# Performance work log

Measured on AMD Instinct MI355X. Metric: run time of the kernel, lower is better.

Reference implementation:

```python
import jax, jax.numpy as jnp
import numpy as np

H = 96  # hidden_dim


def _rbf(dist):
    # GaussianSmearing(start=0, stop=10, num_gaussians=16)
    offset = jnp.linspace(0.0, 10.0, 16, dtype=dist.dtype)
    coeff = -0.5 / (10.0 / 15.0) ** 2
    d = dist[:, None] - offset[None, :]
    return jnp.exp(coeff * d * d)


def _gatv2(s, edge, edge_attr, Wl, bl, Wr, br, We, att, bias):
    # PyG GATv2Conv, heads=1: e = leaky_relu(lin_l(x_src)+lin_r(x_tgt)+lin_edge(ea));
    # alpha = segment_softmax(e @ att, tgt); out = scatter_sum(alpha * lin_l(x_src)) + bias
    N = s.shape[0]
    src, tgt = edge[0], edge[1]
    xl = s @ Wl + bl
    xr = s @ Wr + br
    e = jax.nn.leaky_relu(xl[src] + xr[tgt] + edge_attr @ We, 0.2)  # [E,H]
    logits = e @ att  # [E]
    m = jax.ops.segment_max(logits, tgt, num_segments=N)
    a = jnp.exp(logits - m[tgt])
    denom = jax.ops.segment_sum(a, tgt, num_segments=N)
    alpha = a / denom[tgt]
    out = jax.ops.segment_sum(alpha[:, None] * xl[src], tgt, num_segments=N)
    return out + bias


def _encoder(x, edge, pos, Wemb, bemb, gp):
    s0 = x @ Wemb + bemb                      # [N,H]
    s = jax.nn.silu(s0)
    row, col = edge[0], edge[1]
    dist = jnp.linalg.norm(pos[row] - pos[col], axis=-1)
    ea = _rbf(dist)                           # [E,16]
    s = s + jax.nn.silu(_gatv2(s, edge, ea, *gp))
    v = s0.reshape(x.shape[0], -1, 3)[:, :16, :]  # [N,16,3]
    return s, v


def _forward(x_L, pos_L, x_P, pos_P, edge_L, edge_P, cross_src, cross_tgt,
             Wemb_L, bemb_L, Wl_L, bl_L, Wr_L, br_L, We_L, att_L, bias_L,
             Wemb_P, bemb_P, Wl_P, bl_P, Wr_P, br_P, We_P, att_P, bias_P,
             Win, b_in, Wout, bout, Wq, bq, Wk, bk, Wv, bv, W1, b1, W2, b2):
    s_L, v_L = _encoder(x_L, edge_L, pos_L, Wemb_L, bemb_L,
                        (Wl_L, bl_L, Wr_L, br_L, We_L, att_L, bias_L))
    s_P, v_P = _encoder(x_P, edge_P, pos_P, Wemb_P, bemb_P,
                        (Wl_P, bl_P, Wr_P, br_P, We_P, att_P, bias_P))
    # CausalMolSSM: x + out_proj(silu(in_proj(x)).chunk(2)[0])
    h = jax.nn.silu(s_L @ Win + b_in)[:, : 2 * H]
    s_L = s_L + h @ Wout + bout
    # GVPCrossAttention: per-edge gather, global softmax (dim=0 in source), scatter-add
    q = (s_L @ Wq + bq)[cross_tgt]
    k = (s_P @ Wk + bk)[cross_src]
    logits = jnp.sum(q * k, axis=-1) / 8.0     # [E_X]
    attn = jax.nn.softmax(logits, axis=0)      # global softmax over all edges (as in source)
    vmsg = (s_P @ Wv + bv)[cross_src]
    s_L = s_L.at[cross_tgt].add(attn[:, None] * vmsg)
    # head
    return jax.nn.silu(s_L @ W1 + b1) @ W2 + b2  # v_pred [N_L,3]


def setup_inputs() -> dict:
    N_L, N_P = 8192, 32768
    E_L, E_P, E_X = 262144, 524288, 262144
    D_L, D_P = 167, 21
    ks = iter(jax.random.split(jax.random.key(0), 64))

    def w(shape, fan):
        return (jax.random.normal(next(ks), shape, dtype=jnp.float32) / np.sqrt(fan)).astype(jnp.float32)

    inp = {}
    inp['x_L'] = jax.random.normal(next(ks), (N_L, D_L), dtype=jnp.float32)
    inp['pos_L'] = jax.random.normal(next(ks), (N_L, 3), dtype=jnp.float32)
    inp['x_P'] = jax.random.normal(next(ks), (N_P, D_P), dtype=jnp.float32)
    inp['pos_P'] = jax.random.normal(next(ks), (N_P, 3), dtype=jnp.float32)
    inp['edge_L'] = jax.random.randint(next(ks), (2, E_L), 0, N_L)
    inp['edge_P'] = jax.random.randint(next(ks), (2, E_P), 0, N_P)
    inp['cross_src'] = jax.random.randint(next(ks), (E_X,), 0, N_P)
    inp['cross_tgt'] = jax.random.randint(next(ks), (E_X,), 0, N_L)
    for pre, din in (('L', D_L), ('P', D_P)):
        inp[f'Wemb_{pre}'] = w((din, H), din); inp[f'bemb_{pre}'] = w((H,), din)
        inp[f'Wl_{pre}'] = w((H, H), H); inp[f'bl_{pre}'] = w((H,), H)
        inp[f'Wr_{pre}'] = w((H, H), H); inp[f'br_{pre}'] = w((H,), H)
        inp[f'We_{pre}'] = w((16, H), 16)
        inp[f'att_{pre}'] = w((H,), H)
        inp[f'bias_{pre}'] = w((H,), H)
    inp['Win'] = w((H, 4 * H), H); inp['b_in'] = w((4 * H,), H)
    inp['Wout'] = w((2 * H, H), 2 * H); inp['bout'] = w((H,), 2 * H)
    for n in ('q', 'k', 'v'):
        inp[f'W{n}'] = w((H, H), H); inp[f'b{n}'] = w((H,), H)
    inp['W1'] = w((H, H), H); inp['b1'] = w((H,), H)
    inp['W2'] = w((H, 3), H); inp['b2'] = w((3,), H)
    return inp


def reference(x_L, pos_L, x_P, pos_P, edge_L, edge_P, cross_src, cross_tgt,
              Wemb_L, bemb_L, Wl_L, bl_L, Wr_L, br_L, We_L, att_L, bias_L,
              Wemb_P, bemb_P, Wl_P, bl_P, Wr_P, br_P, We_P, att_P, bias_P,
              Win, b_in, Wout, bout, Wq, bq, Wk, bk, Wv, bv, W1, b1, W2, b2):
    return _forward(x_L, pos_L, x_P, pos_P, edge_L, edge_P, cross_src, cross_tgt,
                    Wemb_L, bemb_L, Wl_L, bl_L, Wr_L, br_L, We_L, att_L, bias_L,
                    Wemb_P, bemb_P, Wl_P, bl_P, Wr_P, br_P, We_P, att_P, bias_P,
                    Win, b_in, Wout, bout, Wq, bq, Wk, bk, Wv, bv, W1, b1, W2, b2)
```

## Files before the change

kernel.cpp:

```cpp
#include <hip/hip_runtime.h>

__device__ __forceinline__ float silu_f(float x) { return x / (1.f + __expf(-x)); }

__device__ __forceinline__ void atomicMaxF(float* addr, float val) {
    if (val >= 0.f) atomicMax((int*)addr, __float_as_int(val));
    else            atomicMin((unsigned int*)addr, __float_as_uint(val));
}

__device__ __forceinline__ unsigned short f2bf(float x) {
    unsigned int u = __float_as_uint(x);
    return (unsigned short)((u + 0x7fffu + ((u >> 16) & 1u)) >> 16);
}
__device__ __forceinline__ float bf2f(unsigned short h) {
    return __uint_as_float(((unsigned int)h) << 16);
}
__device__ __forceinline__ float bf_lo(unsigned int u) { return __uint_as_float(u << 16); }
__device__ __forceinline__ float bf_hi(unsigned int u) { return __uint_as_float(u & 0xffff0000u); }
__device__ __forceinline__ float bfdot(unsigned int a, unsigned int b) {
    return bf_lo(a) * bf_lo(b) + bf_hi(a) * bf_hi(b);
}

__global__ void fill_i(int* __restrict__ p, int v, int n) {
    int i = blockIdx.x * blockDim.x + threadIdx.x;
    if (i < n) p[i] = v;
}

__global__ __launch_bounds__(256) void hist_all_kernel(const int* __restrict__ tgtL,
        const int* __restrict__ tgtP, const int* __restrict__ ctgt, int* __restrict__ count,
        int E_L, int E_P, int E_X, int N_L, int N_P) {
    int e = blockIdx.x * blockDim.x + threadIdx.x;
    if (e < E_L) atomicAdd(&count[tgtL[e]], 1);
    else if (e < E_L + E_P) atomicAdd(&count[N_L + tgtP[e - E_L]], 1);
    else if (e < E_L + E_P + E_X) atomicAdd(&count[N_L + N_P + ctgt[e - E_L - E_P]], 1);
}

__global__ __launch_bounds__(256) void scan_blocksum_kernel(const int* __restrict__ count,
                                                            int* __restrict__ bsum, int n) {
    int b = blockIdx.x, t = threadIdx.x;
    int base = b * 4096 + t * 16;
    int s = 0;
#pragma unroll
    for (int k = 0; k < 16; ++k) {
        int idx = base + k;
        s += (idx < n) ? count[idx] : 0;
    }
#pragma unroll
    for (int off = 1; off < 64; off <<= 1) s += __shfl_xor(s, off, 64);
    __shared__ int ws[4];
    int lane = t & 63, wid = t >> 6;
    if (lane == 0) ws[wid] = s;
    __syncthreads();
    if (t == 0) bsum[b] = ws[0] + ws[1] + ws[2] + ws[3];
}

__global__ void scan_top_kernel(int* __restrict__ bsum, int nb, float* __restrict__ csc) {
    if (threadIdx.x == 0) {
        int run = 0;
        for (int i = 0; i < nb; ++i) { int c = bsum[i]; bsum[i] = run; run += c; }
        csc[0] = -3.4e38f; csc[1] = 0.f;
    }
}

__global__ __launch_bounds__(256) void scan_apply_kernel(const int* __restrict__ count,
        const int* __restrict__ bsum, int* __restrict__ rowptr, int* __restrict__ cursor,
        int n, int E) {
    int b = blockIdx.x, t = threadIdx.x;
    int base = b * 4096 + t * 16;
    int v[16];
    int s = 0;
#pragma unroll
    for (int k = 0; k < 16; ++k) {
        int idx = base + k;
        v[k] = (idx < n) ? count[idx] : 0;
        s += v[k];
    }
    int lane = t & 63, wid = t >> 6;
    int inc = s;
#pragma unroll
    for (int off = 1; off < 64; off <<= 1) {
        int o = __shfl_up(inc, off, 64);
        if (lane >= off) inc += o;
    }
    __shared__ int ws[4];
    if (lane == 63) ws[wid] = inc;
    __syncthreads();
    int woff = 0;
    for (int w = 0; w < wid; ++w) woff += ws[w];
    int prefix = bsum[b] + woff + (inc - s);
#pragma unroll
    for (int k = 0; k < 16; ++k) {
        int idx = base + k;
        if (idx < n) { rowptr[idx] = prefix; cursor[idx] = prefix; prefix += v[k]; }
    }
    if (b == 0 && t == 0) rowptr[n] = E;
}

__global__ __launch_bounds__(256) void pre_all_kernel(const int* __restrict__ eL,
        const int* __restrict__ eP, const int* __restrict__ csrc, const int* __restrict__ ctgt,
        const float* __restrict__ posL, const float* __restrict__ posP,
        int* __restrict__ cursor, unsigned int* __restrict__ sdp,
        int E_L, int E_P, int E_X, int N_L, int N_P) {
    int e = blockIdx.x * blockDim.x + threadIdx.x;
    if (e >= E_L + E_P + E_X) return;
    unsigned int pack;
    int node;
    if (e < E_L + E_P) {
        const int* ed; const float* pos; int idx, E, nbase;
        if (e < E_L) { ed = eL; pos = posL; idx = e; E = E_L; nbase = 0; }
        else         { ed = eP; pos = posP; idx = e - E_L; E = E_P; nbase = N_L; }
        int si = ed[idx], ti = ed[E + idx];
        node = nbase + ti;
        float dx = pos[si * 3 + 0] - pos[ti * 3 + 0];
        float dy = pos[si * 3 + 1] - pos[ti * 3 + 1];
        float dz = pos[si * 3 + 2] - pos[ti * 3 + 2];
        float dist = sqrtf(dx * dx + dy * dy + dz * dz);
        int dq = min((int)(dist * 4096.f), 65535);
        pack = (unsigned int)(si + nbase) | ((unsigned int)dq << 16);
    } else {
        int idx = e - E_L - E_P;
        int ti = ctgt[idx];
        pack = (unsigned int)csrc[idx] | ((unsigned int)ti << 16);
        node = N_L + N_P + ti;
    }
    int p = atomicAdd(&cursor[node], 1);
    sdp[p] = pack;
}

__global__ __launch_bounds__(96) void rbf_table_pack_kernel(const float* __restrict__ We_L,
        const float* __restrict__ We_P, unsigned int* __restrict__ T2_L,
        unsigned int* __restrict__ T2_P) {
    int b = blockIdx.x;
    const float* We = (b < 1024) ? We_L : We_P;
    unsigned int* T2 = (b < 1024) ? T2_L : T2_P;
    int i = (b < 1024) ? b : b - 1024;
    int h = threadIdx.x;
    float d0 = (float)i * 0.015625f, d1 = (float)(i + 1) * 0.015625f;
    float a0 = 0.f, a1 = 0.f;
#pragma unroll
    for (int g = 0; g < 16; ++g) {
        float w = We[g * 96 + h];
        float t0 = d0 - 0.66666667f * (float)g;
        float t1 = d1 - 0.66666667f * (float)g;
        a0 += __expf(-1.125f * t0 * t0) * w;
        a1 += __expf(-1.125f * t1 * t1) * w;
    }
    T2[i * 96 + h] = (unsigned int)f2bf(a0) | ((unsigned int)f2bf(a1 - a0) << 16);
}

__global__ __launch_bounds__(256) void gat_all_kernel(const int* __restrict__ rowptr,
        const unsigned int* __restrict__ sdp, const unsigned short* __restrict__ xlb,
        const unsigned short* __restrict__ xrb,
        const unsigned int* __restrict__ T2_L, const unsigned int* __restrict__ T2_P,
        const float* __restrict__ att_L, const float* __restrict__ att_P,
        const float* __restrict__ bias_L, const float* __restrict__ bias_P,
        float* __restrict__ s_L, float* __restrict__ s_P, int N_L, int Ncomb) {
    int tid = threadIdx.x;
    int l = tid & 31;
    int n = blockIdx.x * 8 + (tid >> 5);
    if (n >= Ncomb) return;
    bool isL = n < N_L;
    const unsigned int* T2 = isL ? T2_L : T2_P;
    const float* att = isL ? att_L : att_P;
    const float* bias = isL ? bias_L : bias_P;
    float* srow = isL ? (s_L + (size_t)n * 96) : (s_P + (size_t)(n - N_L) * 96);
    float att0 = att[l], att1 = att[32 + l], att2 = att[64 + l];
    size_t nb = (size_t)n * 96;
    float xr0 = bf2f(xrb[nb + l]), xr1 = bf2f(xrb[nb + 32 + l]), xr2 = bf2f(xrb[nb + 64 + l]);
    int beg = rowptr[n], end = rowptr[n + 1];
    float m = -3.4e38f, d = 0.f, a0 = 0.f, a1 = 0.f, a2 = 0.f;
    for (int j = beg; j < end; j += 4) {
        unsigned int tp0[4], tp1[4], tp2[4];
        unsigned short xs0[4], xs1[4], xs2[4];
        float ff[4];
#pragma unroll
        for (int k = 0; k < 4; ++k) {
            int jj = min(j + k, end - 1);
            unsigned int u = sdp[jj];
            int src = (int)(u & 0xffffu);
            int dq = (int)(u >> 16);
            int i = dq >> 6;
            ff[k] = (float)(dq & 63) * 0.015625f;
            const unsigned int* tr = T2 + (size_t)i * 96;
            tp0[k] = tr[l]; tp1[k] = tr[32 + l]; tp2[k] = tr[64 + l];
            const unsigned short* xp = xlb + (size_t)src * 96;
            xs0[k] = xp[l]; xs1[k] = xp[32 + l]; xs2[k] = xp[64 + l];
        }
        float y0[4], y1[4], y2[4], lt[4];
#pragma unroll
        for (int k = 0; k < 4; ++k) {
            y0[k] = bf2f(xs0[k]); y1[k] = bf2f(xs1[k]); y2[k] = bf2f(xs2[k]);
            float v0 = y0[k] + xr0 + bf_lo(tp0[k]) + ff[k] * bf_hi(tp0[k]);
            float v1 = y1[k] + xr1 + bf_lo(tp1[k]) + ff[k] * bf_hi(tp1[k]);
            float v2 = y2[k] + xr2 + bf_lo(tp2[k]) + ff[k] * bf_hi(tp2[k]);
            v0 = fmaxf(v0, 0.f) + 0.2f * fminf(v0, 0.f);
            v1 = fmaxf(v1, 0.f) + 0.2f * fminf(v1, 0.f);
            v2 = fmaxf(v2, 0.f) + 0.2f * fminf(v2, 0.f);
            float t = v0 * att0 + v1 * att1 + v2 * att2;
#pragma unroll
            for (int off = 1; off < 32; off <<= 1) t += __shfl_xor(t, off, 64);
            lt[k] = (j + k < end) ? t : -3.4e38f;
        }
        float bm = fmaxf(fmaxf(lt[0], lt[1]), fmaxf(lt[2], lt[3]));
        float nm = fmaxf(m, bm);
        float sc = __expf(m - nm);
        d *= sc; a0 *= sc; a1 *= sc; a2 *= sc;
#pragma unroll
        for (int k = 0; k < 4; ++k) {
            float w = __expf(lt[k] - nm);
            d += w;
            a0 += w * y0[k]; a1 += w * y1[k]; a2 += w * y2[k];
        }
        m = nm;
    }
    float agg0 = (d > 0.f) ? a0 / d : 0.f;
    float agg1 = (d > 0.f) ? a1 / d : 0.f;
    float agg2 = (d > 0.f) ? a2 / d : 0.f;
    srow[l]      += silu_f(agg0 + bias[l]);
    srow[32 + l] += silu_f(agg1 + bias[32 + l]);
    srow[64 + l] += silu_f(agg2 + bias[64 + l]);
}

__global__ __launch_bounds__(256) void cross_logit_e_kernel(const unsigned int* __restrict__ sdX,
        const unsigned short* __restrict__ qnb, const unsigned short* __restrict__ knb,
        float* __restrict__ clog_s, float* __restrict__ csc, int E) {
    int e = blockIdx.x * blockDim.x + threadIdx.x;
    float logit = -3.4e38f;
    if (e < E) {
        unsigned int u = sdX[e];
        int src = (int)(u & 0xffffu);
        int tgt = (int)(u >> 16);
        const uint4* q4 = (const uint4*)(qnb + (size_t)tgt * 96);
        const uint4* k4 = (const uint4*)(knb + (size_t)src * 96);
        float acc = 0.f;
#pragma unroll
        for (int i = 0; i < 12; ++i) {
            uint4 qa = q4[i], ka = k4[i];
            acc += bfdot(qa.x, ka.x) + bfdot(qa.y, ka.y) + bfdot(qa.z, ka.z) + bfdot(qa.w, ka.w);
        }
        logit = acc * 0.125f;
        clog_s[e] = logit;
    }
    __shared__ float red[256];
    red[threadIdx.x] = logit; __syncthreads();
    for (int s = 128; s > 0; s >>= 1) {
        if (threadIdx.x < s) red[threadIdx.x] = fmaxf(red[threadIdx.x], red[threadIdx.x + s]);
        __syncthreads();
    }
    if (threadIdx.x == 0) atomicMaxF(&csc[0], red[0]);
}

__global__ __launch_bounds__(256) void cross_denom_kernel(const float* __restrict__ clog_s,
                                                          float* __restrict__ csc, int E) {
    int e = blockIdx.x * blockDim.x + threadIdx.x;
    float a = 0.f;
    float mg = csc[0];
    if (e < E) a = __expf(clog_s[e] - mg);
    __shared__ float red[256];
    red[threadIdx.x] = a; __syncthreads();
    for (int s = 128; s > 0; s >>= 1) {
        if (threadIdx.x < s) red[threadIdx.x] += red[threadIdx.x + s];
        __syncthreads();
    }
    if (threadIdx.x == 0) atomicAdd(&csc[1], red[0]);
}

__global__ __launch_bounds__(256) void cross_apply_v4_kernel(const int* __restrict__ rowptr,
        const unsigned int* __restrict__ sdp, const float* __restrict__ clog_s,
        const unsigned short* __restrict__ vnb, const float* __restrict__ csc,
        float* __restrict__ sL, int N, int baseX) {
    int tid = threadIdx.x;
    int l = tid & 31;
    int n = blockIdx.x * 8 + (tid >> 5);
    if (n >= N) return;
    int beg = rowptr[n], end = rowptr[n + 1];
    if (beg == end) return;
    float M = csc[0], invD = 1.f / csc[1];
    float a0 = 0.f, a1 = 0.f, a2 = 0.f;
    for (int j = beg; j < end; j += 4) {
        unsigned short v0[4], v1[4], v2[4]; float w[4];
#pragma unroll
        for (int k = 0; k < 4; ++k) {
            int jj = min(j + k, end - 1);
            int src = (int)(sdp[jj] & 0xffffu);
            const unsigned short* vp = vnb + (size_t)src * 96;
            v0[k] = vp[l]; v1[k] = vp[32 + l]; v2[k] = vp[64 + l];
            w[k] = (j + k < end) ? __expf(clog_s[jj - baseX] - M) : 0.f;
        }
#pragma unroll
        for (int k = 0; k < 4; ++k) {
            a0 += w[k] * bf2f(v0[k]); a1 += w[k] * bf2f(v1[k]); a2 += w[k] * bf2f(v2[k]);
        }
    }
    size_t nb = (size_t)n * 96;
    sL[nb + l]      += a0 * invD;
    sL[nb + 32 + l] += a1 * invD;
    sL[nb + 64 + l] += a2 * invD;
}


__global__ __launch_bounds__(192) void enc_all_kernel(
        const float* __restrict__ x_L, const float* __restrict__ x_P,
        const float* __restrict__ WembL, const float* __restrict__ bembL,
        const float* __restrict__ WembP, const float* __restrict__ bembP,
        const float* __restrict__ WlL, const float* __restrict__ blL,
        const float* __restrict__ WrL, const float* __restrict__ brL,
        const float* __restrict__ WlP, const float* __restrict__ blP,
        const float* __restrict__ WrP, const float* __restrict__ brP,
        float* __restrict__ s_L, float* __restrict__ s_P,
        unsigned short* __restrict__ xlb, unsigned short* __restrict__ xrb,
        int N_L, int N_P, int D_L, int D_P, int BL) {
    __shared__ float xs[32 * 167];
    __shared__ float ss[32 * 96];
    int b = blockIdx.x;
    bool isL = b < BL;
    const float* x    = isL ? x_L : x_P;
    const float* Wemb = isL ? WembL : WembP;
    const float* bemb = isL ? bembL : bembP;
    const float* Wl   = isL ? WlL : WlP;
    const float* bl   = isL ? blL : blP;
    const float* Wr   = isL ? WrL : WrP;
    const float* br   = isL ? brL : brP;
    float* sOut = isL ? s_L : s_P;
    int N = isL ? N_L : N_P;
    int D = isL ? D_L : D_P;
    int n0 = (isL ? b : b - BL) * 32;
    int cbase = isL ? 0 : N_L;
    int t = threadIdx.x;
    int hg = t % 24, h4 = hg * 4;
    int rg = t / 24;
    for (int i = t; i < 32 * D; i += 192) {
        int r = i / D, dd = i - r * D, nn = n0 + r;
        xs[i] = (nn < N) ? x[(size_t)nn * D + dd] : 0.f;
    }
    __syncthreads();
    float4 be = *(const float4*)&bemb[h4];
    float acc[4][4];
#pragma unroll
    for (int r = 0; r < 4; ++r) { acc[r][0] = be.x; acc[r][1] = be.y; acc[r][2] = be.z; acc[r][3] = be.w; }
    const float* xrow = &xs[rg * 4 * D];
    for (int dd = 0; dd < D; ++dd) {
        float4 w = *(const float4*)&Wemb[dd * 96 + h4];
#pragma unroll
        for (int r = 0; r < 4; ++r) {
            float xv = xrow[r * D + dd];
            acc[r][0] += xv * w.x; acc[r][1] += xv * w.y;
            acc[r][2] += xv * w.z; acc[r][3] += xv * w.w;
        }
    }
#pragma unroll
    for (int r = 0; r < 4; ++r) {
        int row = rg * 4 + r, nn = n0 + row;
        float4 v = make_float4(silu_f(acc[r][0]), silu_f(acc[r][1]),
                               silu_f(acc[r][2]), silu_f(acc[r][3]));
        *(float4*)&ss[row * 96 + h4] = v;
        if (nn < N) *(float4*)&sOut[(size_t)nn * 96 + h4] = v;
    }
    __syncthreads();
    float4 b1v = *(const float4*)&bl[h4];
    float4 b2v = *(const float4*)&br[h4];
    float a1[4][4], a2[4][4];
#pragma unroll
    for (int r = 0; r < 4; ++r) {
        a1[r][0] = b1v.x; a1[r][1] = b1v.y; a1[r][2] = b1v.z; a1[r][3] = b1v.w;
        a2[r][0] = b2v.x; a2[r][1] = b2v.y; a2[r][2] = b2v.z; a2[r][3] = b2v.w;
    }
    const float* srow = &ss[rg * 4 * 96];
    for (int k = 0; k < 96; ++k) {
        float4 w1 = *(const float4*)&Wl[k * 96 + h4];
        float4 w2 = *(const float4*)&Wr[k * 96 + h4];
#pragma unroll
        for (int r = 0; r < 4; ++r) {
            float xv = srow[r * 96 + k];
            a1[r][0] += xv * w1.x; a1[r][1] += xv * w1.y; a1[r][2] += xv * w1.z; a1[r][3] += xv * w1.w;
            a2[r][0] += xv * w2.x; a2[r][1] += xv * w2.y; a2[r][2] += xv * w2.z; a2[r][3] += xv * w2.w;
        }
    }
#pragma unroll
    for (int r = 0; r < 4; ++r) {
        int nn = n0 + rg * 4 + r;
        if (nn < N) {
            size_t o = (size_t)(cbase + nn) * 96 + h4;
            *(ushort4*)&xlb[o] = make_ushort4(f2bf(a1[r][0]), f2bf(a1[r][1]), f2bf(a1[r][2]), f2bf(a1[r][3]));
            *(ushort4*)&xrb[o] = make_ushort4(f2bf(a2[r][0]), f2bf(a2[r][1]), f2bf(a2[r][2]), f2bf(a2[r][3]));
        }
    }
}

__global__ __launch_bounds__(192) void qkv_all_kernel(
        const float* __restrict__ s_L, const float* __restrict__ s_P,
        const float* __restrict__ Wq, const float* __restrict__ bq,
        const float* __restrict__ Wk, const float* __restrict__ bk,
        const float* __restrict__ Wv, const float* __restrict__ bv,
        unsigned short* __restrict__ qnb, unsigned short* __restrict__ knb,
        unsigned short* __restrict__ vnb, int N_L, int N_P, int BL) {
    __shared__ float xs[32 * 96];
    int b = blockIdx.x;
    bool isL = b < BL;
    const float* s = isL ? s_L : s_P;
    int N = isL ? N_L : N_P;
    int n0 = (isL ? b : b - BL) * 32;
    int t = threadIdx.x;
    int hg = t % 24, h4 = hg * 4;
    int rg = t / 24;
    for (int i = t; i < 32 * 96; i += 192) {
        int r = i / 96, c = i - r * 96, nn = n0 + r;
        xs[i] = (nn < N) ? s[(size_t)nn * 96 + c] : 0.f;
    }
    __syncthreads();
    const float* srow = &xs[rg * 4 * 96];
    if (isL) {
        float4 bb = *(const float4*)&bq[h4];
        float a1[4][4];
#pragma unroll
        for (int r = 0; r < 4; ++r) { a1[r][0] = bb.x; a1[r][1] = bb.y; a1[r][2] = bb.z; a1[r][3] = bb.w; }
        for (int k = 0; k < 96; ++k) {
            float4 w = *(const float4*)&Wq[k * 96 + h4];
#pragma unroll
            for (int r = 0; r < 4; ++r) {
                float xv = srow[r * 96 + k];
                a1[r][0] += xv * w.x; a1[r][1] += xv * w.y; a1[r][2] += xv * w.z; a1[r][3] += xv * w.w;
            }
        }
#pragma unroll
        for (int r = 0; r < 4; ++r) {
            int nn = n0 + rg * 4 + r;
            if (nn < N)
                *(ushort4*)&qnb[(size_t)nn * 96 + h4] =
                    make_ushort4(f2bf(a1[r][0]), f2bf(a1[r][1]), f2bf(a1[r][2]), f2bf(a1[r][3]));
        }
    } else {
        float4 bb1 = *(const float4*)&bk[h4];
        float4 bb2 = *(const float4*)&bv[h4];
        float a1[4][4], a2[4][4];
#pragma unroll
        for (int r = 0; r < 4; ++r) {
            a1[r][0] = bb1.x; a1[r][1] = bb1.y; a1[r][2] = bb1.z; a1[r][3] = bb1.w;
            a2[r][0] = bb2.x; a2[r][1] = bb2.y; a2[r][2] = bb2.z; a2[r][3] = bb2.w;
        }
        for (int k = 0; k < 96; ++k) {
            float4 w1 = *(const float4*)&Wk[k * 96 + h4];
            float4 w2 = *(const float4*)&Wv[k * 96 + h4];
#pragma unroll
            for (int r = 0; r < 4; ++r) {
                float xv = srow[r * 96 + k];
                a1[r][0] += xv * w1.x; a1[r][1] += xv * w1.y; a1[r][2] += xv * w1.z; a1[r][3] += xv * w1.w;
                a2[r][0] += xv * w2.x; a2[r][1] += xv * w2.y; a2[r][2] += xv * w2.z; a2[r][3] += xv * w2.w;
            }
        }
#pragma unroll
        for (int r = 0; r < 4; ++r) {
            int nn = n0 + rg * 4 + r;
            if (nn < N) {
                *(ushort4*)&knb[(size_t)nn * 96 + h4] =
                    make_ushort4(f2bf(a1[r][0]), f2bf(a1[r][1]), f2bf(a1[r][2]), f2bf(a1[r][3]));
                *(ushort4*)&vnb[(size_t)nn * 96 + h4] =
                    make_ushort4(f2bf(a2[r][0]), f2bf(a2[r][1]), f2bf(a2[r][2]), f2bf(a2[r][3]));
            }
        }
    }
}

__global__ __launch_bounds__(192) void ssm3_kernel(float* __restrict__ sL,
        const float* __restrict__ Win, const float* __restrict__ b_in,
        const float* __restrict__ Wout, const float* __restrict__ bout, int N) {
    __shared__ float row[8 * 96];
    __shared__ float u[8 * 192];
    int t = threadIdx.x;
    int n0 = blockIdx.x * 8;
    for (int i = t; i < 8 * 96; i += 192) {
        int r = i / 96, c = i - r * 96, nn = n0 + r;
        row[i] = (nn < N) ? sL[(size_t)nn * 96 + c] : 0.f;
    }
    __syncthreads();
    {
        int cg = t % 48, c4 = cg * 4;
        int rg = t / 48;
        float4 bb = *(const float4*)&b_in[c4];
        float a[2][4];
#pragma unroll
        for (int r = 0; r < 2; ++r) { a[r][0] = bb.x; a[r][1] = bb.y; a[r][2] = bb.z; a[r][3] = bb.w; }
        const float* rr = &row[rg * 2 * 96];
        for (int k = 0; k < 96; ++k) {
            float4 w = *(const float4*)&Win[k * 384 + c4];
#pragma unroll
            for (int r = 0; r < 2; ++r) {
                float xv = rr[r * 96 + k];
                a[r][0] += xv * w.x; a[r][1] += xv * w.y; a[r][2] += xv * w.z; a[r][3] += xv * w.w;
            }
        }
#pragma unroll
        for (int r = 0; r < 2; ++r) {
            int ro = rg * 2 + r;
            u[ro * 192 + c4 + 0] = silu_f(a[r][0]);
            u[ro * 192 + c4 + 1] = silu_f(a[r][1]);
            u[ro * 192 + c4 + 2] = silu_f(a[r][2]);
            u[ro * 192 + c4 + 3] = silu_f(a[r][3]);
        }
    }
    __syncthreads();
    {
        int hg = t % 24, h4 = hg * 4;
        int rg2 = t / 24;
        float4 bb = *(const float4*)&bout[h4];
        float a[4] = {bb.x, bb.y, bb.z, bb.w};
        const float* ur = &u[rg2 * 192];
        for (int j = 0; j < 192; ++j) {
            float4 w = *(const float4*)&Wout[j * 96 + h4];
            float uv = ur[j];
            a[0] += uv * w.x; a[1] += uv * w.y; a[2] += uv * w.z; a[3] += uv * w.w;
        }
        int nn = n0 + rg2;
        if (nn < N) {
            float4 rv = *(const float4*)&row[rg2 * 96 + h4];
            *(float4*)&sL[(size_t)nn * 96 + h4] =
                make_float4(rv.x + a[0], rv.y + a[1], rv.z + a[2], rv.w + a[3]);
        }
    }
}

__global__ __launch_bounds__(192) void head3_kernel(const float* __restrict__ sL,
        const float* __restrict__ W1, const float* __restrict__ b1,
        const float* __restrict__ W2, const float* __restrict__ b2,
        float* __restrict__ out, int N) {
    __shared__ float buf[32 * 96];
    __shared__ float tt[32 * 96];
    int t = threadIdx.x;
    int n0 = blockIdx.x * 32;
    for (int i = t; i < 32 * 96; i += 192) {
        int r = i / 96, c = i - r * 96, nn = n0 + r;
        buf[i] = (nn < N) ? sL[(size_t)nn * 96 + c] : 0.f;
    }
    __syncthreads();
    int hg = t % 24, h4 = hg * 4;
    int rg = t / 24;
    float4 bb = *(const float4*)&b1[h4];
    float a[4][4];
#pragma unroll
    for (int r = 0; r < 4; ++r) { a[r][0] = bb.x; a[r][1] = bb.y; a[r][2] = bb.z; a[r][3] = bb.w; }
    const float* srow = &buf[rg * 4 * 96];
    for (int k = 0; k < 96; ++k) {
        float4 w = *(const float4*)&W1[k * 96 + h4];
#pragma unroll
        for (int r = 0; r < 4; ++r) {
            float xv = srow[r * 96 + k];
            a[r][0] += xv * w.x; a[r][1] += xv * w.y; a[r][2] += xv * w.z; a[r][3] += xv * w.w;
        }
    }
#pragma unroll
    for (int r = 0; r < 4; ++r) {
        int row = rg * 4 + r;
        *(float4*)&tt[row * 96 + h4] = make_float4(silu_f(a[r][0]), silu_f(a[r][1]),
                                                   silu_f(a[r][2]), silu_f(a[r][3]));
    }
    __syncthreads();
    if (t < 96) {
        int r = t / 3, c = t - r * 3;
        float o = b2[c];
        const float* tr = &tt[r * 96];
        for (int j = 0; j < 96; ++j) o += tr[j] * W2[j * 3 + c];
        int nn = n0 + r;
        if (nn < N) out[nn * 3 + c] = o;
    }
}

static inline int cdiv(int a, int b) { return (a + b - 1) / b; }

extern "C" void kernel_launch(void* const* d_in, const int* in_sizes, int n_in,
                              void* d_out, int out_size, void* d_ws, size_t ws_size,
                              hipStream_t stream) {
    const float* x_L   = (const float*)d_in[0];
    const float* pos_L = (const float*)d_in[1];
    const float* x_P   = (const float*)d_in[2];
    const float* pos_P = (const float*)d_in[3];
    const int* edge_L = (const int*)d_in[4];
    const int* edge_P = (const int*)d_in[5];
    const int* csrc   = (const int*)d_in[6];
    const int* ctgt   = (const int*)d_in[7];
    const float *Wemb_L = (const float*)d_in[8],  *bemb_L = (const float*)d_in[9];
    const float *Wl_L = (const float*)d_in[10], *bl_L = (const float*)d_in[11];
    const float *Wr_L = (const float*)d_in[12], *br_L = (const float*)d_in[13];
    const float *We_L = (const float*)d_in[14], *att_L = (const float*)d_in[15], *bias_L = (const float*)d_in[16];
    const float *Wemb_P = (const float*)d_in[17], *bemb_P = (const float*)d_in[18];
    const float *Wl_P = (const float*)d_in[19], *bl_P = (const float*)d_in[20];
    const float *Wr_P = (const float*)d_in[21], *br_P = (const float*)d_in[22];
    const float *We_P = (const float*)d_in[23], *att_P = (const float*)d_in[24], *bias_P = (const float*)d_in[25];
    const float *Win = (const float*)d_in[26], *b_in = (const float*)d_in[27];
    const float *Wout = (const float*)d_in[28], *bout = (const float*)d_in[29];
    const float *Wq = (const float*)d_in[30], *bq = (const float*)d_in[31];
    const float *Wk = (const float*)d_in[32], *bk = (const float*)d_in[33];
    const float *Wv = (const float*)d_in[34], *bv = (const float*)d_in[35];
    const float *W1 = (const float*)d_in[36], *b1 = (const float*)d_in[37];
    const float *W2 = (const float*)d_in[38], *b2 = (const float*)d_in[39];

    const int N_L = in_sizes[1] / 3;
    const int N_P = in_sizes[3] / 3;
    const int E_L = in_sizes[4] / 2;
    const int E_P = in_sizes[5] / 2;
    const int E_X = in_sizes[6];
    const int D_L = in_sizes[0] / N_L;
    const int D_P = in_sizes[2] / N_P;
    const int Ncomb = N_L + N_P;
    const int Ntot = N_L + N_P + N_L;
    const int Etot = E_L + E_P + E_X;
    const int baseX = E_L + E_P;

    float* ws = (float*)d_ws;
    float*          s_L    = ws;
    float*          s_P    = s_L + (size_t)N_L * 96;
    unsigned short* xrb    = (unsigned short*)(s_P + (size_t)N_P * 96);
    unsigned short* xlb    = xrb + (size_t)Ncomb * 96;
    unsigned short* knb    = xlb + (size_t)Ncomb * 96;
    unsigned short* vnb    = knb + (size_t)N_P * 96;
    unsigned short* qnb    = vnb + (size_t)N_P * 96;
    unsigned int*   sdp    = (unsigned int*)(qnb + (size_t)N_L * 96);
    float*          clog_s = (float*)(sdp + (size_t)Etot);
    unsigned int*   T2_L   = (unsigned int*)(clog_s + (size_t)E_X);
    unsigned int*   T2_P   = T2_L + 1024 * 96;
    int*            rowptr = (int*)(T2_P + 1024 * 96);
    int*            count  = rowptr + (size_t)Ntot + 1;
    int*            cursor = count + (size_t)Ntot;
    float*          csc    = (float*)(cursor + (size_t)Ntot);
    int*            bsum   = (int*)(csc + 2);

    const int BL = cdiv(N_L, 32), BP = cdiv(N_P, 32);

    rbf_table_pack_kernel<<<2048, 96, 0, stream>>>(We_L, We_P, T2_L, T2_P);
    fill_i<<<cdiv(Ntot, 256), 256, 0, stream>>>(count, 0, Ntot);
    hist_all_kernel<<<cdiv(Etot, 256), 256, 0, stream>>>(edge_L + E_L, edge_P + E_P, ctgt,
        count, E_L, E_P, E_X, N_L, N_P);
    scan_blocksum_kernel<<<cdiv(Ntot, 4096), 256, 0, stream>>>(count, bsum, Ntot);
    scan_top_kernel<<<1, 64, 0, stream>>>(bsum, cdiv(Ntot, 4096), csc);
    scan_apply_kernel<<<cdiv(Ntot, 4096), 256, 0, stream>>>(count, bsum, rowptr, cursor, Ntot, Etot);
    pre_all_kernel<<<cdiv(Etot, 256), 256, 0, stream>>>(edge_L, edge_P, csrc, ctgt,
        pos_L, pos_P, cursor, sdp, E_L, E_P, E_X, N_L, N_P);

    enc_all_kernel<<<BL + BP, 192, 0, stream>>>(x_L, x_P, Wemb_L, bemb_L, Wemb_P, bemb_P,
        Wl_L, bl_L, Wr_L, br_L, Wl_P, bl_P, Wr_P, br_P,
        s_L, s_P, xlb, xrb, N_L, N_P, D_L, D_P, BL);

    gat_all_kernel<<<cdiv(Ncomb, 8), 256, 0, stream>>>(rowptr, sdp, xlb, xrb, T2_L, T2_P,
        att_L, att_P, bias_L, bias_P, s_L, s_P, N_L, Ncomb);

    ssm3_kernel<<<cdiv(N_L, 8), 192, 0, stream>>>(s_L, Win, b_in, Wout, bout, N_L);

    qkv_all_kernel<<<BL + BP, 192, 0, stream>>>(s_L, s_P, Wq, bq, Wk, bk, Wv, bv,
        qnb, knb, vnb, N_L, N_P, BL);
    cross_logit_e_kernel<<<cdiv(E_X, 256), 256, 0, stream>>>(sdp + (size_t)baseX, qnb, knb,
        clog_s, csc, E_X);
    cross_denom_kernel<<<cdiv(E_X, 256), 256, 0, stream>>>(clog_s, csc, E_X);
    cross_apply_v4_kernel<<<cdiv(N_L, 8), 256, 0, stream>>>(rowptr + N_L + N_P, sdp,
        clog_s, vnb, csc, s_L, N_L, baseX);

    head3_kernel<<<cdiv(N_L, 32), 192, 0, stream>>>(s_L, W1, b1, W2, b2, (float*)d_out, N_L);
}
```

Before: 466.5 us.

## Vectorize per-lane feature gathers and pad shared-memory rows to avoid bank conflicts

The GAT and cross-attention apply kernels now give each lane two adjacent features in one 32-bit or 64-bit load, plus a third scalar feature, instead of three strided 16-bit loads. Several GEMM-style kernels pad shared-memory rows from 96 to 100 floats to spread row accesses across banks. The encoder kernel reuses its input staging buffer instead of a second shared array, which lowers LDS use. It also swaps three divisions for one reciprocal and writes the SSM intermediate with float4 stores. The wider gathers reduce memory instructions in the gather-bound kernels, but the lane-to-feature mapping changes, so outputs land in a different but equivalent order.

```diff
diff --git a/kernel.cpp b/kernel.cpp
--- a/kernel.cpp
+++ b/kernel.cpp
@@ -163,14 +163,16 @@
     const float* att = isL ? att_L : att_P;
     const float* bias = isL ? bias_L : bias_P;
     float* srow = isL ? (s_L + (size_t)n * 96) : (s_P + (size_t)(n - N_L) * 96);
-    float att0 = att[l], att1 = att[32 + l], att2 = att[64 + l];
+    int h01 = 2 * l, h2 = 64 + l;
+    float att0 = att[h01], att1 = att[h01 + 1], att2 = att[h2];
     size_t nb = (size_t)n * 96;
-    float xr0 = bf2f(xrb[nb + l]), xr1 = bf2f(xrb[nb + 32 + l]), xr2 = bf2f(xrb[nb + 64 + l]);
+    unsigned int xru = *(const unsigned int*)&xrb[nb + h01];
+    float xr0 = bf_lo(xru), xr1 = bf_lo(xru >> 16), xr2 = bf2f(xrb[nb + h2]);
     int beg = rowptr[n], end = rowptr[n + 1];
     float m = -3.4e38f, d = 0.f, a0 = 0.f, a1 = 0.f, a2 = 0.f;
     for (int j = beg; j < end; j += 4) {
-        unsigned int tp0[4], tp1[4], tp2[4];
-        unsigned short xs0[4], xs1[4], xs2[4];
+        uint2 tpA[4]; unsigned int tp2[4];
+        unsigned int xA[4]; unsigned short x2[4];
         float ff[4];
 #pragma unroll
         for (int k = 0; k < 4; ++k) {
@@ -181,16 +183,18 @@
             int i = dq >> 6;
             ff[k] = (float)(dq & 63) * 0.015625f;
             const unsigned int* tr = T2 + (size_t)i * 96;
-            tp0[k] = tr[l]; tp1[k] = tr[32 + l]; tp2[k] = tr[64 + l];
+            tpA[k] = *(const uint2*)&tr[h01];
+            tp2[k] = tr[h2];
             const unsigned short* xp = xlb + (size_t)src * 96;
-            xs0[k] = xp[l]; xs1[k] = xp[32 + l]; xs2[k] = xp[64 + l];
+            xA[k] = *(const unsigned int*)&xp[h01];
+            x2[k] = xp[h2];
         }
         float y0[4], y1[4], y2[4], lt[4];
 #pragma unroll
         for (int k = 0; k < 4; ++k) {
-            y0[k] = bf2f(xs0[k]); y1[k] = bf2f(xs1[k]); y2[k] = bf2f(xs2[k]);
-            float v0 = y0[k] + xr0 + bf_lo(tp0[k]) + ff[k] * bf_hi(tp0[k]);
-            float v1 = y1[k] + xr1 + bf_lo(tp1[k]) + ff[k] * bf_hi(tp1[k]);
+            y0[k] = bf_lo(xA[k]); y1[k] = bf_lo(xA[k] >> 16); y2[k] = bf2f(x2[k]);
+            float v0 = y0[k] + xr0 + bf_lo(tpA[k].x) + ff[k] * bf_hi(tpA[k].x);
+            float v1 = y1[k] + xr1 + bf_lo(tpA[k].y) + ff[k] * bf_hi(tpA[k].y);
             float v2 = y2[k] + xr2 + bf_lo(tp2[k]) + ff[k] * bf_hi(tp2[k]);
             v0 = fmaxf(v0, 0.f) + 0.2f * fminf(v0, 0.f);
             v1 = fmaxf(v1, 0.f) + 0.2f * fminf(v1, 0.f);
@@ -212,12 +216,10 @@
         }
         m = nm;
     }
-    float agg0 = (d > 0.f) ? a0 / d : 0.f;
-    float agg1 = (d > 0.f) ? a1 / d : 0.f;
-    float agg2 = (d > 0.f) ? a2 / d : 0.f;
-    srow[l]      += silu_f(agg0 + bias[l]);
-    srow[32 + l] += silu_f(agg1 + bias[32 + l]);
-    srow[64 + l] += silu_f(agg2 + bias[64 + l]);
+    float inv = (d > 0.f) ? 1.f / d : 0.f;
+    srow[h01]     += silu_f(a0 * inv + bias[h01]);
+    srow[h01 + 1] += silu_f(a1 * inv + bias[h01 + 1]);
+    srow[h2]      += silu_f(a2 * inv + bias[h2]);
 }
 
 __global__ __launch_bounds__(256) void cross_logit_e_kernel(const unsigned int* __restrict__ sdX,
@@ -274,27 +276,29 @@
     if (n >= N) return;
     int beg = rowptr[n], end = rowptr[n + 1];
     if (beg == end) return;
+    int h01 = 2 * l, h2 = 64 + l;
     float M = csc[0], invD = 1.f / csc[1];
     float a0 = 0.f, a1 = 0.f, a2 = 0.f;
     for (int j = beg; j < end; j += 4) {
-        unsigned short v0[4], v1[4], v2[4]; float w[4];
+        unsigned int vA[4]; unsigned short v2[4]; float w[4];
 #pragma unroll
         for (int k = 0; k < 4; ++k) {
             int jj = min(j + k, end - 1);
             int src = (int)(sdp[jj] & 0xffffu);
             const unsigned short* vp = vnb + (size_t)src * 96;
-            v0[k] = vp[l]; v1[k] = vp[32 + l]; v2[k] = vp[64 + l];
+            vA[k] = *(const unsigned int*)&vp[h01];
+            v2[k] = vp[h2];
             w[k] = (j + k < end) ? __expf(clog_s[jj - baseX] - M) : 0.f;
         }
 #pragma unroll
         for (int k = 0; k < 4; ++k) {
-            a0 += w[k] * bf2f(v0[k]); a1 += w[k] * bf2f(v1[k]); a2 += w[k] * bf2f(v2[k]);
+            a0 += w[k] * bf_lo(vA[k]); a1 += w[k] * bf_lo(vA[k] >> 16); a2 += w[k] * bf2f(v2[k]);
         }
     }
     size_t nb = (size_t)n * 96;
-    sL[nb + l]      += a0 * invD;
-    sL[nb + 32 + l] += a1 * invD;
-    sL[nb + 64 + l] += a2 * invD;
+    sL[nb + h01]     += a0 * invD;
+    sL[nb + h01 + 1] += a1 * invD;
+    sL[nb + h2]      += a2 * invD;
 }
 
 
@@ -310,7 +314,6 @@
         unsigned short* __restrict__ xlb, unsigned short* __restrict__ xrb,
         int N_L, int N_P, int D_L, int D_P, int BL) {
     __shared__ float xs[32 * 167];
-    __shared__ float ss[32 * 96];
     int b = blockIdx.x;
     bool isL = b < BL;
     const float* x    = isL ? x_L : x_P;
@@ -347,12 +350,13 @@
             acc[r][2] += xv * w.z; acc[r][3] += xv * w.w;
         }
     }
+    __syncthreads();
 #pragma unroll
     for (int r = 0; r < 4; ++r) {
         int row = rg * 4 + r, nn = n0 + row;
         float4 v = make_float4(silu_f(acc[r][0]), silu_f(acc[r][1]),
                                silu_f(acc[r][2]), silu_f(acc[r][3]));
-        *(float4*)&ss[row * 96 + h4] = v;
+        *(float4*)&xs[row * 100 + h4] = v;
         if (nn < N) *(float4*)&sOut[(size_t)nn * 96 + h4] = v;
     }
     __syncthreads();
@@ -364,13 +368,13 @@
         a1[r][0] = b1v.x; a1[r][1] = b1v.y; a1[r][2] = b1v.z; a1[r][3] = b1v.w;
         a2[r][0] = b2v.x; a2[r][1] = b2v.y; a2[r][2] = b2v.z; a2[r][3] = b2v.w;
     }
-    const float* srow = &ss[rg * 4 * 96];
+    const float* srow = &xs[rg * 4 * 100];
     for (int k = 0; k < 96; ++k) {
         float4 w1 = *(const float4*)&Wl[k * 96 + h4];
         float4 w2 = *(const float4*)&Wr[k * 96 + h4];
 #pragma unroll
         for (int r = 0; r < 4; ++r) {
-            float xv = srow[r * 96 + k];
+            float xv = srow[r * 100 + k];
             a1[r][0] += xv * w1.x; a1[r][1] += xv * w1.y; a1[r][2] += xv * w1.z; a1[r][3] += xv * w1.w;
             a2[r][0] += xv * w2.x; a2[r][1] += xv * w2.y; a2[r][2] += xv * w2.z; a2[r][3] += xv * w2.w;
         }
@@ -393,7 +397,7 @@
         const float* __restrict__ Wv, const float* __restrict__ bv,
         unsigned short* __restrict__ qnb, unsigned short* __restrict__ knb,
         unsigned short* __restrict__ vnb, int N_L, int N_P, int BL) {
-    __shared__ float xs[32 * 96];
+    __shared__ float xs[32 * 100];
     int b = blockIdx.x;
     bool isL = b < BL;
     const float* s = isL ? s_L : s_P;
@@ -404,10 +408,10 @@
     int rg = t / 24;
     for (int i = t; i < 32 * 96; i += 192) {
         int r = i / 96, c = i - r * 96, nn = n0 + r;
-        xs[i] = (nn < N) ? s[(size_t)nn * 96 + c] : 0.f;
-    }
-    __syncthreads();
-    const float* srow = &xs[rg * 4 * 96];
+        xs[r * 100 + c] = (nn < N) ? s[(size_t)nn * 96 + c] : 0.f;
+    }
+    __syncthreads();
+    const float* srow = &xs[rg * 4 * 100];
     if (isL) {
         float4 bb = *(const float4*)&bq[h4];
         float a1[4][4];
@@ -417,7 +421,7 @@
             float4 w = *(const float4*)&Wq[k * 96 + h4];
 #pragma unroll
             for (int r = 0; r < 4; ++r) {
-                float xv = srow[r * 96 + k];
+                float xv = srow[r * 100 + k];
                 a1[r][0] += xv * w.x; a1[r][1] += xv * w.y; a1[r][2] += xv * w.z; a1[r][3] += xv * w.w;
             }
         }
@@ -442,7 +446,7 @@
             float4 w2 = *(const float4*)&Wv[k * 96 + h4];
 #pragma unroll
             for (int r = 0; r < 4; ++r) {
-                float xv = srow[r * 96 + k];
+                float xv = srow[r * 100 + k];
                 a1[r][0] += xv * w1.x; a1[r][1] += xv * w1.y; a1[r][2] += xv * w1.z; a1[r][3] += xv * w1.w;
                 a2[r][0] += xv * w2.x; a2[r][1] += xv * w2.y; a2[r][2] += xv * w2.z; a2[r][3] += xv * w2.w;
             }
@@ -463,13 +467,13 @@
 __global__ __launch_bounds__(192) void ssm3_kernel(float* __restrict__ sL,
         const float* __restrict__ Win, const float* __restrict__ b_in,
         const float* __restrict__ Wout, const float* __restrict__ bout, int N) {
-    __shared__ float row[8 * 96];
-    __shared__ float u[8 * 192];
+    __shared__ float row[8 * 100];
+    __shared__ float u[8 * 196];
     int t = threadIdx.x;
     int n0 = blockIdx.x * 8;
     for (int i = t; i < 8 * 96; i += 192) {
         int r = i / 96, c = i - r * 96, nn = n0 + r;
-        row[i] = (nn < N) ? sL[(size_t)nn * 96 + c] : 0.f;
+        row[r * 100 + c] = (nn < N) ? sL[(size_t)nn * 96 + c] : 0.f;
     }
     __syncthreads();
     {
@@ -479,22 +483,20 @@
         float a[2][4];
 #pragma unroll
         for (int r = 0; r < 2; ++r) { a[r][0] = bb.x; a[r][1] = bb.y; a[r][2] = bb.z; a[r][3] = bb.w; }
-        const float* rr = &row[rg * 2 * 96];
+        const float* rr = &row[rg * 2 * 100];
         for (int k = 0; k < 96; ++k) {
             float4 w = *(const float4*)&Win[k * 384 + c4];
 #pragma unroll
             for (int r = 0; r < 2; ++r) {
-                float xv = rr[r * 96 + k];
+                float xv = rr[r * 100 + k];
                 a[r][0] += xv * w.x; a[r][1] += xv * w.y; a[r][2] += xv * w.z; a[r][3] += xv * w.w;
             }
         }
 #pragma unroll
         for (int r = 0; r < 2; ++r) {
             int ro = rg * 2 + r;
-            u[ro * 192 + c4 + 0] = silu_f(a[r][0]);
-            u[ro * 192 + c4 + 1] = silu_f(a[r][1]);
-            u[ro * 192 + c4 + 2] = silu_f(a[r][2]);
-            u[ro * 192 + c4 + 3] = silu_f(a[r][3]);
+            *(float4*)&u[ro * 196 + c4] = make_float4(silu_f(a[r][0]), silu_f(a[r][1]),
+                                                      silu_f(a[r][2]), silu_f(a[r][3]));
         }
     }
     __syncthreads();
@@ -503,7 +505,7 @@
         int rg2 = t / 24;
         float4 bb = *(const float4*)&bout[h4];
         float a[4] = {bb.x, bb.y, bb.z, bb.w};
-        const float* ur = &u[rg2 * 192];
+        const float* ur = &u[rg2 * 196];
         for (int j = 0; j < 192; ++j) {
             float4 w = *(const float4*)&Wout[j * 96 + h4];
             float uv = ur[j];
@@ -511,7 +513,7 @@
         }
         int nn = n0 + rg2;
         if (nn < N) {
-            float4 rv = *(const float4*)&row[rg2 * 96 + h4];
+            float4 rv = *(const float4*)&row[rg2 * 100 + h4];
             *(float4*)&sL[(size_t)nn * 96 + h4] =
                 make_float4(rv.x + a[0], rv.y + a[1], rv.z + a[2], rv.w + a[3]);
         }
@@ -522,13 +524,13 @@
         const float* __restrict__ W1, const float* __restrict__ b1,
         const float* __restrict__ W2, const float* __restrict__ b2,
         float* __restrict__ out, int N) {
-    __shared__ float buf[32 * 96];
-    __shared__ float tt[32 * 96];
+    __shared__ float buf[32 * 100];
+    __shared__ float tt[32 * 100];
     int t = threadIdx.x;
     int n0 = blockIdx.x * 32;
     for (int i = t; i < 32 * 96; i += 192) {
         int r = i / 96, c = i - r * 96, nn = n0 + r;
-        buf[i] = (nn < N) ? sL[(size_t)nn * 96 + c] : 0.f;
+        buf[r * 100 + c] = (nn < N) ? sL[(size_t)nn * 96 + c] : 0.f;
     }
     __syncthreads();
     int hg = t % 24, h4 = hg * 4;
@@ -537,26 +539,26 @@
     float a[4][4];
 #pragma unroll
     for (int r = 0; r < 4; ++r) { a[r][0] = bb.x; a[r][1] = bb.y; a[r][2] = bb.z; a[r][3] = bb.w; }
-    const float* srow = &buf[rg * 4 * 96];
+    const float* srow = &buf[rg * 4 * 100];
     for (int k = 0; k < 96; ++k) {
         float4 w = *(const float4*)&W1[k * 96 + h4];
 #pragma unroll
         for (int r = 0; r < 4; ++r) {
-            float xv = srow[r * 96 + k];
+            float xv = srow[r * 100 + k];
             a[r][0] += xv * w.x; a[r][1] += xv * w.y; a[r][2] += xv * w.z; a[r][3] += xv * w.w;
         }
     }
 #pragma unroll
     for (int r = 0; r < 4; ++r) {
         int row = rg * 4 + r;
-        *(float4*)&tt[row * 96 + h4] = make_float4(silu_f(a[r][0]), silu_f(a[r][1]),
-                                                   silu_f(a[r][2]), silu_f(a[r][3]));
+        *(float4*)&tt[row * 100 + h4] = make_float4(silu_f(a[r][0]), silu_f(a[r][1]),
+                                                    silu_f(a[r][2]), silu_f(a[r][3]));
     }
     __syncthreads();
     if (t < 96) {
         int r = t / 3, c = t - r * 3;
         float o = b2[c];
-        const float* tr = &tt[r * 96];
+        const float* tr = &tt[r * 100];
         for (int j = 0; j < 96; ++j) o += tr[j] * W2[j * 3 + c];
         int nn = n0 + r;
         if (nn < N) out[nn * 3 + c] = o;
```

New measurement: 478.5 us. 1.03x slower.
